# Kernel tuning notes

Measured on AMD Instinct MI355X. Metric: run time of the kernel, lower is better.

Reference implementation:

```python
import jax, jax.numpy as jnp
import numpy as np

B, T, F, D, NH, HD, WIN = 4, 512, 32, 128, 4, 32, 64
HIDDEN = 4 * D


def _ln(x, g, b, eps=1e-5):
    m = x.mean(-1, keepdims=True)
    v = ((x - m) ** 2).mean(-1, keepdims=True)
    return (x - m) / jnp.sqrt(v + eps) * g + b


def _rope(x):
    # x: [N, T, NH, HD] -- identical rotary applied to every head (matches per-head loop)
    hd = x.shape[-1]
    inv_freq = 1.0 / (10000.0 ** (jnp.arange(0, hd, 2, dtype=jnp.float32) / hd))
    t = jnp.arange(x.shape[1], dtype=jnp.float32)
    fr = t[:, None] * inv_freq                      # [T, HD/2]
    sin = jnp.sin(fr)[None, :, None, :]
    cos = jnp.cos(fr)[None, :, None, :]
    xe, xo = x[..., 0::2], x[..., 1::2]
    re = xe * cos - xo * sin
    ro = xe * sin + xo * cos
    return jnp.stack([re, ro], axis=-1).reshape(x.shape)


def setup_inputs() -> dict:
    key = jax.random.key(0)
    ks = jax.random.split(key, 8)
    s = 0.05
    return {
        "x": jax.random.normal(ks[0], (B, T, F), jnp.float32),
        "W_in": jax.random.normal(ks[1], (D, F), jnp.float32) * s,
        "b_in": jnp.zeros((D,), jnp.float32),
        "gamma1": jnp.ones((D,), jnp.float32),
        "beta1": jnp.zeros((D,), jnp.float32),
        "gamma2": jnp.ones((D,), jnp.float32),
        "beta2": jnp.zeros((D,), jnp.float32),
        "W_qkv": jax.random.normal(ks[2], (3 * D, D), jnp.float32) * s,
        "b_qkv": jnp.zeros((3 * D,), jnp.float32),
        "W_o": jax.random.normal(ks[3], (D, D), jnp.float32) * s,
        "b_o": jnp.zeros((D,), jnp.float32),
        "W1": jax.random.normal(ks[4], (HIDDEN, D), jnp.float32) * s,
        "b1": jnp.zeros((HIDDEN,), jnp.float32),
        "W2": jax.random.normal(ks[5], (D, HIDDEN), jnp.float32) * s,
        "b2": jnp.zeros((D,), jnp.float32),
        "W_out": jax.random.normal(ks[6], (F, D), jnp.float32) * s,
        "b_out": jnp.zeros((F,), jnp.float32),
    }


def reference(x, W_in, b_in, gamma1, beta1, gamma2, beta2, W_qkv, b_qkv,
              W_o, b_o, W1, b1, W2, b2, W_out, b_out):
    Bb, Tt, Ff = x.shape
    # channel-independent projection: hcf[b,f,t,:] = x[b,t,f] * W_in[:,f] + b_in
    hcf = jnp.einsum('btf,df->bftd', x, W_in) + b_in        # [B,F,T,D]
    hcf = hcf.reshape(Bb * Ff, Tt, D)                       # [BF,T,D]
    h1 = _ln(hcf, gamma1, beta1)
    # RoPE on q,k BEFORE the attention's internal qkv projection (as in source)
    qk = _rope(h1.reshape(Bb * Ff, Tt, NH, HD)).reshape(Bb * Ff, Tt, D)
    Wq, Wk, Wv = jnp.split(W_qkv, 3, axis=0)
    bq, bk, bv = jnp.split(b_qkv, 3)
    Q = (qk @ Wq.T + bq).reshape(-1, Tt, NH, HD)
    K = (qk @ Wk.T + bk).reshape(-1, Tt, NH, HD)
    V = (h1 @ Wv.T + bv).reshape(-1, Tt, NH, HD)
    i = jnp.arange(Tt)
    allowed = (i[None, :] <= i[:, None]) & ((i[:, None] - i[None, :]) <= WIN)
    mask = jnp.where(allowed, 0.0, -jnp.inf)                # [T,T]
    scores = jnp.einsum('bthd,bshd->bhts', Q, K) / jnp.sqrt(jnp.float32(HD)) + mask
    p = jax.nn.softmax(scores, axis=-1)
    o = jnp.einsum('bhts,bshd->bthd', p, V).reshape(-1, Tt, D)
    y = o @ W_o.T + b_o
    h2 = hcf + y
    h3 = _ln(h2, gamma2, beta2)
    ffn = jax.nn.gelu(h3 @ W1.T + b1, approximate=False) @ W2.T + b2
    h4 = h2 + ffn
    y_out = h4.reshape(Bb, Ff, Tt, D).mean(-1).transpose(0, 2, 1)   # [B,T,F]
    y_proj = (x @ W_in.T + b_in) @ W_out.T + b_out                   # [B,T,F]
    return x + y_out + y_proj
```

## Files before the change

kernel.cpp:

```cpp
#include <hip/hip_runtime.h>
#include <hip/hip_bf16.h>

typedef unsigned short u16;
typedef unsigned int u32;
typedef __attribute__((ext_vector_type(8))) short bf16x8;
typedef __attribute__((ext_vector_type(8))) unsigned short u16x8;
typedef __attribute__((ext_vector_type(4))) float f32x4;
typedef __attribute__((ext_vector_type(4))) unsigned short u16x4;

static constexpr int TSEQ = 512;
static constexpr int NSEQ = 128;
static constexpr int NTOK = NSEQ * TSEQ;

__device__ __forceinline__ float bf2f(u16 u) {
  u32 i = ((u32)u) << 16; float f; __builtin_memcpy(&f, &i, 4); return f;
}
__device__ __forceinline__ u16 f2bf(float f) {
  u32 u; __builtin_memcpy(&u, &f, 4);
  return (u16)((u + 0x7FFFu + ((u >> 16) & 1u)) >> 16);
}
__device__ __forceinline__ f32x4 mfma16(bf16x8 a, bf16x8 b, f32x4 c) {
  return __builtin_amdgcn_mfma_f32_16x16x32_bf16(a, b, c, 0, 0, 0);
}
__device__ __forceinline__ void gload_lds16(const u16* g, u16* l) {
  __builtin_amdgcn_global_load_lds((const __attribute__((address_space(1))) void*)g,
                                   (__attribute__((address_space(3))) void*)l, 16, 0, 0);
}
__device__ __forceinline__ float gelu_t(float v) {
  float uu = 0.7978845608f * (v + 0.044715f * v * v * v);
  return v * __builtin_amdgcn_rcpf(1.f + __expf(-2.f * uu));
}

__global__ void k0_prep(const float* __restrict__ Wqkv, const float* __restrict__ Wo,
                        const float* __restrict__ W1, const float* __restrict__ W2,
                        const float* __restrict__ b2,
                        const float* __restrict__ W_in, const float* __restrict__ b_in,
                        const float* __restrict__ Wout, const float* __restrict__ bout,
                        u16* __restrict__ Wqkv_b, u16* __restrict__ Wo_b,
                        u16* __restrict__ W1_b, float* __restrict__ cm,
                        float* __restrict__ b2m,
                        float* __restrict__ Wcomb, float* __restrict__ bcomb,
                        float* __restrict__ rc, float* __restrict__ rs) {
  int i = blockIdx.x * 256 + threadIdx.x;
  if (i < 49152) Wqkv_b[i] = f2bf(Wqkv[i]);
  if (i < 16384) Wo_b[i] = f2bf(Wo[i]);
  if (i < 65536) W1_b[i] = f2bf(W1[i]);
  if (i < 512) {
    float s = 0.f;
    for (int d = 0; d < 128; ++d) s += W2[d * 512 + i];
    cm[i] = s * (1.f / 128.f);
  }
  if (i == 0) {
    float s = 0.f;
    for (int d = 0; d < 128; ++d) s += b2[d];
    *b2m = s * (1.f / 128.f);
  }
  if (i < 1024) {
    int l = i >> 5, f = i & 31;
    float s = 0.f;
    for (int d = 0; d < 128; ++d) s += Wout[l * 128 + d] * W_in[d * 32 + f];
    Wcomb[i] = s;
  }
  if (i < 32) {
    float s = bout[i];
    for (int d = 0; d < 128; ++d) s += Wout[i * 128 + d] * b_in[d];
    bcomb[i] = s;
  }
  if (i < 8192) {
    int t = i >> 4, fi = i & 15;
    float inv = powf(10000.f, -(float)(2 * fi) / 32.f);
    float ang = (float)t * inv;
    rc[i] = cosf(ang); rs[i] = sinf(ang);
  }
}

__global__ __launch_bounds__(512, 4)
void embed_qkv(const float* __restrict__ x, const float* __restrict__ W_in,
               const float* __restrict__ b_in,
               const float* __restrict__ g1, const float* __restrict__ be1,
               const float* __restrict__ rc, const float* __restrict__ rs,
               const u16* __restrict__ Wqkv, const float* __restrict__ bqkv,
               u16* __restrict__ QKb, u16* __restrict__ Vb) {
  __shared__ u16 Aq[64 * 128];
  __shared__ u16 Ah[64 * 128];
  const int tid = threadIdx.x, l = tid & 63, w = tid >> 6;
  const int lr = l & 15, lg = l >> 4;
  const int m0 = blockIdx.x * 64;
  const int seq = m0 >> 9, f = seq & 31, b = seq >> 5, tbase = m0 & 511;

  {
    const int tok = tid >> 3, j = tid & 7, d0 = j * 16;
    const int t = tbase + tok;
    float xv = x[((b << 9) + t) * 32 + f];
    float hc[16], av[16];
    float s = 0.f, ss = 0.f;
    #pragma unroll
    for (int m = 0; m < 16; ++m) {
      float v = xv * W_in[(d0 + m) * 32 + f] + b_in[d0 + m];
      hc[m] = v; s += v; ss += v * v;
    }
    s += __shfl_xor(s, 1); ss += __shfl_xor(ss, 1);
    s += __shfl_xor(s, 2); ss += __shfl_xor(ss, 2);
    s += __shfl_xor(s, 4); ss += __shfl_xor(ss, 4);
    float mean = s * (1.f / 128.f);
    float var = ss * (1.f / 128.f) - mean * mean;
    float rstd = rsqrtf(var + 1e-5f);
    #pragma unroll
    for (int m = 0; m < 16; ++m)
      av[m] = (hc[m] - mean) * rstd * g1[d0 + m] + be1[d0 + m];
    u16x8 ah0, ah1, aq0, aq1;
    #pragma unroll
    for (int m = 0; m < 8; ++m) { ah0[m] = f2bf(av[m]); ah1[m] = f2bf(av[8 + m]); }
    #pragma unroll
    for (int m = 0; m < 8; ++m) {
      int i16 = ((d0 >> 1) + m) & 15;
      float c = rc[t * 16 + i16], sn = rs[t * 16 + i16];
      float re = av[2 * m] * c - av[2 * m + 1] * sn;
      float ro = av[2 * m] * sn + av[2 * m + 1] * c;
      if (m < 4) { aq0[2 * m] = f2bf(re); aq0[2 * m + 1] = f2bf(ro); }
      else { aq1[2 * (m - 4)] = f2bf(re); aq1[2 * (m - 4) + 1] = f2bf(ro); }
    }
    const int p0 = j * 2;
    const int s0 = p0 ^ (tok & 7), s1 = (p0 + 1) ^ (tok & 7);
    *(u16x8*)(Ah + (tok * 16 + s0) * 8) = ah0;
    *(u16x8*)(Ah + (tok * 16 + s1) * 8) = ah1;
    *(u16x8*)(Aq + (tok * 16 + s0) * 8) = aq0;
    *(u16x8*)(Aq + (tok * 16 + s1) * 8) = aq1;
  }
  __syncthreads();

  #pragma unroll 1
  for (int ph = 0; ph < 3; ++ph) {
    const u16* As = (ph == 2) ? Ah : Aq;
    const int wrow = ph * 128 + w * 16;
    const u16* wr = Wqkv + (size_t)(wrow + lr) * 128 + lg * 8;
    bf16x8 wf0 = *(const bf16x8*)(wr);
    bf16x8 wf1 = *(const bf16x8*)(wr + 32);
    bf16x8 wf2 = *(const bf16x8*)(wr + 64);
    bf16x8 wf3 = *(const bf16x8*)(wr + 96);
    f32x4 bs = *(const f32x4*)(bqkv + wrow + lg * 4);
    u16* C = (ph == 2) ? Vb : QKb;
    const int ldc = (ph == 2) ? 128 : 256;
    const int ccol = ((ph == 2) ? 0 : ph * 128) + w * 16 + lg * 4;
    #pragma unroll
    for (int tt = 0; tt < 4; ++tt) {
      const int tok = tt * 16 + lr;
      const u16* ar = As + (tok * 16) * 8;
      f32x4 a0 = mfma16(wf0, *(const bf16x8*)(ar + ((lg ^ (lr & 7)) << 3)),
                        (f32x4){0.f, 0.f, 0.f, 0.f});
      a0 = mfma16(wf1, *(const bf16x8*)(ar + (((4 + lg) ^ (lr & 7)) << 3)), a0);
      f32x4 a1 = mfma16(wf2, *(const bf16x8*)(ar + (((8 + lg) ^ (lr & 7)) << 3)),
                        (f32x4){0.f, 0.f, 0.f, 0.f});
      a1 = mfma16(wf3, *(const bf16x8*)(ar + (((12 + lg) ^ (lr & 7)) << 3)), a1);
      f32x4 a = a0 + a1;
      u16x4 qv;
      #pragma unroll
      for (int r = 0; r < 4; ++r) qv[r] = f2bf(a[r] + bs[r]);
      *(u16x4*)(C + (size_t)(m0 + tok) * ldc + ccol) = qv;
    }
    __builtin_amdgcn_sched_barrier(0);
  }
}

__global__ __launch_bounds__(512, 4)
void wo_ln_ffn(const u16* __restrict__ OB, const u16* __restrict__ Wo_b,
               const float* __restrict__ bo,
               const float* __restrict__ x, const float* __restrict__ W_in,
               const float* __restrict__ b_in,
               const float* __restrict__ g2, const float* __restrict__ be2,
               const u16* __restrict__ W1b, const float* __restrict__ b1,
               const float* __restrict__ cm, const float* __restrict__ b2m,
               float* __restrict__ yout) {
  __shared__ u16 Buf[64 * 136];
  __shared__ float Sm[64 * 9], Sq[64 * 9];
  __shared__ float Yp[64 * 9];
  __shared__ float Hm[64];
  __shared__ float Xs[64];
  const int tid = threadIdx.x, l = tid & 63, w = tid >> 6;
  const int lr = l & 15, lg = l >> 4;
  const int m0 = blockIdx.x * 64;
  const int seq = m0 >> 9, f = seq & 31, b = seq >> 5, tbase = m0 & 511;
  const int wb = __builtin_amdgcn_readfirstlane(tid & 0x1C0);

  #pragma unroll
  for (int it = 0; it < 2; ++it) {
    int ci = it * 512 + tid;
    int row = ci >> 4, p = ci & 15;
    gload_lds16(OB + (size_t)(m0 + row) * 128 + ((p ^ (row & 7)) << 3),
                Buf + (size_t)(it * 512 + wb) * 8);
  }
  if (tid < 64) Xs[tid] = x[((b << 9) + tbase + tid) * 32 + f];
  __syncthreads();

  const int wrow = w * 16;
  {
    const u16* wr0 = Wo_b + (size_t)(wrow + lr) * 128 + lg * 8;
    bf16x8 wf0 = *(const bf16x8*)(wr0);
    bf16x8 wf1 = *(const bf16x8*)(wr0 + 32);
    bf16x8 wf2 = *(const bf16x8*)(wr0 + 64);
    bf16x8 wf3 = *(const bf16x8*)(wr0 + 96);
    f32x4 bs = *(const f32x4*)(bo + wrow + lg * 4);
    f32x4 winc, binc;
    #pragma unroll
    for (int r = 0; r < 4; ++r) {
      winc[r] = W_in[(wrow + lg * 4 + r) * 32 + f];
      binc[r] = b_in[wrow + lg * 4 + r];
    }
    f32x4 hv[4];
    #pragma unroll
    for (int tt = 0; tt < 4; ++tt) {
      const int tok = tt * 16 + lr;
      const u16* ar = Buf + (tok * 16) * 8;
      f32x4 a0 = mfma16(wf0, *(const bf16x8*)(ar + ((lg ^ (lr & 7)) << 3)),
                        (f32x4){0.f, 0.f, 0.f, 0.f});
      a0 = mfma16(wf1, *(const bf16x8*)(ar + (((4 + lg) ^ (lr & 7)) << 3)), a0);
      f32x4 a1 = mfma16(wf2, *(const bf16x8*)(ar + (((8 + lg) ^ (lr & 7)) << 3)),
                        (f32x4){0.f, 0.f, 0.f, 0.f});
      a1 = mfma16(wf3, *(const bf16x8*)(ar + (((12 + lg) ^ (lr & 7)) << 3)), a1);
      f32x4 a = a0 + a1;
      float xv = Xs[tok];
      #pragma unroll
      for (int r = 0; r < 4; ++r)
        hv[tt][r] = a[r] + bs[r] + (xv * winc[r] + binc[r]);
    }
    #pragma unroll
    for (int tt = 0; tt < 4; ++tt) {
      float psm = hv[tt][0] + hv[tt][1] + hv[tt][2] + hv[tt][3];
      float psq = hv[tt][0] * hv[tt][0] + hv[tt][1] * hv[tt][1]
                + hv[tt][2] * hv[tt][2] + hv[tt][3] * hv[tt][3];
      psm += __shfl_xor(psm, 16); psq += __shfl_xor(psq, 16);
      psm += __shfl_xor(psm, 32); psq += __shfl_xor(psq, 32);
      if (lg == 0) { Sm[(tt * 16 + lr) * 9 + w] = psm; Sq[(tt * 16 + lr) * 9 + w] = psq; }
    }
    __syncthreads();
    f32x4 gm = *(const f32x4*)(g2 + wrow + lg * 4);
    f32x4 bt = *(const f32x4*)(be2 + wrow + lg * 4);
    #pragma unroll
    for (int tt = 0; tt < 4; ++tt) {
      const int tok = tt * 16 + lr;
      float s = 0.f, q = 0.f;
      #pragma unroll
      for (int ww = 0; ww < 8; ++ww) { s += Sm[tok * 9 + ww]; q += Sq[tok * 9 + ww]; }
      float mean = s * (1.f / 128.f);
      float var = q * (1.f / 128.f) - mean * mean;
      float rstd = rsqrtf(var + 1e-5f);
      if (w == 0 && lg == 0) Hm[tok] = mean;
      u16x4 qv;
      #pragma unroll
      for (int r = 0; r < 4; ++r)
        qv[r] = f2bf((hv[tt][r] - mean) * rstd * gm[r] + bt[r]);
      *(u16x4*)(Buf + tok * 136 + wrow + lg * 4) = qv;
    }
  }
  __syncthreads();

  float yacc[4] = {0.f, 0.f, 0.f, 0.f};
  #pragma unroll 1
  for (int p = 0; p < 4; ++p) {
    const int hb = (p * 8 + w) * 16;
    const u16* wr = W1b + (size_t)(hb + lr) * 128 + lg * 8;
    bf16x8 wf0 = *(const bf16x8*)(wr);
    bf16x8 wf1 = *(const bf16x8*)(wr + 32);
    bf16x8 wf2 = *(const bf16x8*)(wr + 64);
    bf16x8 wf3 = *(const bf16x8*)(wr + 96);
    f32x4 cmv = *(const f32x4*)(cm + hb + lg * 4);
    f32x4 bsv = *(const f32x4*)(b1 + hb + lg * 4);
    #pragma unroll
    for (int tt = 0; tt < 4; ++tt) {
      const u16* ar = Buf + (tt * 16 + lr) * 136 + lg * 8;
      f32x4 a0 = mfma16(wf0, *(const bf16x8*)(ar), (f32x4){0.f, 0.f, 0.f, 0.f});
      a0 = mfma16(wf1, *(const bf16x8*)(ar + 32), a0);
      f32x4 a1 = mfma16(wf2, *(const bf16x8*)(ar + 64), (f32x4){0.f, 0.f, 0.f, 0.f});
      a1 = mfma16(wf3, *(const bf16x8*)(ar + 96), a1);
      f32x4 a = a0 + a1;
      #pragma unroll
      for (int r = 0; r < 4; ++r)
        yacc[tt] += cmv[r] * gelu_t(a[r] + bsv[r]);
    }
    __builtin_amdgcn_sched_barrier(0);
  }

  #pragma unroll
  for (int tt = 0; tt < 4; ++tt) {
    float p = yacc[tt];
    p += __shfl_xor(p, 16);
    p += __shfl_xor(p, 32);
    if (lg == 0) Yp[(tt * 16 + lr) * 9 + w] = p;
  }
  __syncthreads();
  if (tid < 64) {
    float s = 0.f;
    #pragma unroll
    for (int ww = 0; ww < 8; ++ww) s += Yp[tid * 9 + ww];
    yout[m0 + tid] = Hm[tid] + b2m[0] + s;
  }
}

__global__ __launch_bounds__(256, 4)
void attn_mfma(const u16* __restrict__ QK, const u16* __restrict__ V, u16* __restrict__ O) {
  __shared__ u16 Ks[192 * 32];
  __shared__ u16 Vt[32 * 192];
  __shared__ u16 Pl[4][16 * 96];
  typedef __attribute__((ext_vector_type(2))) unsigned int u32x2;
  const int qstart = blockIdx.x * 128, seq = blockIdx.y, h = blockIdx.z;
  const int tid = threadIdx.x, w = tid >> 6, l = tid & 63;
  const int lr = l & 15, lg = l >> 4;
  const size_t base = (size_t)seq * TSEQ;

  #pragma unroll
  for (int it = 0; it < 3; ++it) {
    int idx = it * 256 + tid;
    int kl = idx >> 2, c = idx & 3;
    int kg = qstart - 64 + kl; if (kg < 0) kg = 0;
    bf16x8 kv = *(const bf16x8*)(QK + (base + kg) * 256 + 128 + h * 32 + c * 8);
    int pc = c ^ ((kl >> 1) & 3);
    *(bf16x8*)(Ks + kl * 32 + pc * 8) = kv;
    bf16x8 vv = *(const bf16x8*)(V + (base + kg) * 128 + h * 32 + c * 8);
    #pragma unroll
    for (int j = 0; j < 8; ++j) {
      int hd = c * 8 + j;
      int f = ((hd & 7) ^ (hd >> 3)) & 7;
      Vt[hd * 192 + (((kl >> 3) ^ f) * 8) + (kl & 7)] = (u16)vv[j];
    }
  }
  __syncthreads();

  const float scale = 0.17677669529663687f;
  for (int qt = 0; qt < 2; ++qt) {
    const int klbase = (w * 2 + qt) * 16;
    const int t0 = qstart + klbase;
    bf16x8 qf = *(const bf16x8*)(QK + (base + t0 + lr) * 256 + h * 32 + lg * 8);
    f32x4 s[5];
    #pragma unroll
    for (int kt = 0; kt < 5; ++kt) {
      int key = klbase + kt * 16 + lr;
      int pc = lg ^ ((key >> 1) & 3);
      bf16x8 kf = *(const bf16x8*)(Ks + key * 32 + pc * 8);
      s[kt] = mfma16(kf, qf, (f32x4){0.f, 0.f, 0.f, 0.f});
    }
    float m = -1e30f;
    #pragma unroll
    for (int kt = 0; kt < 5; ++kt)
      #pragma unroll
      for (int r = 0; r < 4; ++r) {
        int kl = kt * 16 + lg * 4 + r;
        bool valid = (kl >= lr) && (kl <= lr + 64) && (kl >= 64 - t0);
        float sv = valid ? s[kt][r] * scale : -1e30f;
        s[kt][r] = sv;
        m = fmaxf(m, sv);
      }
    m = fmaxf(m, __shfl_xor(m, 16));
    m = fmaxf(m, __shfl_xor(m, 32));
    float sum = 0.f;
    #pragma unroll
    for (int kt = 0; kt < 5; ++kt)
      #pragma unroll
      for (int r = 0; r < 4; ++r) { float p = __expf(s[kt][r] - m); s[kt][r] = p; sum += p; }
    sum += __shfl_xor(sum, 16);
    sum += __shfl_xor(sum, 32);
    float rinv = 1.f / sum;
    u16* P = Pl[w];
    #pragma unroll
    for (int kt = 0; kt < 5; ++kt) {
      u32 lo = (u32)f2bf(s[kt][0] * rinv) | ((u32)f2bf(s[kt][1] * rinv) << 16);
      u32 hi = (u32)f2bf(s[kt][2] * rinv) | ((u32)f2bf(s[kt][3] * rinv) << 16);
      int u = 2 * kt + (lg >> 1);
      int up = (u & ~3) | ((u & 3) ^ (lr & 3));
      *(u32x2*)(P + lr * 96 + up * 8 + (lg & 1) * 4) = (u32x2){lo, hi};
    }
    {
      int u = 10 + (lg >> 1);
      int up = (u & ~3) | ((u & 3) ^ (lr & 3));
      *(u32x2*)(P + lr * 96 + up * 8 + (lg & 1) * 4) = (u32x2){0u, 0u};
    }
    f32x4 acc[2] = {{0.f,0.f,0.f,0.f},{0.f,0.f,0.f,0.f}};
    #pragma unroll
    for (int c = 0; c < 3; ++c) {
      int u = 4 * c + (lg ^ (lr & 3));
      bf16x8 pf = *(const bf16x8*)(P + lr * 96 + u * 8);
      #pragma unroll
      for (int n = 0; n < 2; ++n) {
        int hd = n * 16 + lr;
        int f = ((hd & 7) ^ (hd >> 3)) & 7;
        int uv = (klbase >> 3) + 4 * c + lg; if (uv > 23) uv = 23;
        bf16x8 vf = *(const bf16x8*)(Vt + hd * 192 + ((uv ^ f) * 8));
        acc[n] = mfma16(pf, vf, acc[n]);
      }
    }
    #pragma unroll
    for (int n = 0; n < 2; ++n)
      #pragma unroll
      for (int r = 0; r < 4; ++r)
        O[(base + t0 + lg * 4 + r) * 128 + h * 32 + n * 16 + lr] = f2bf(acc[n][r]);
  }
}

__global__ void k7_out(const float* __restrict__ x, const float* __restrict__ Wcomb,
                       const float* __restrict__ bcomb, const float* __restrict__ yout,
                       float* __restrict__ out) {
  __shared__ float Wc[32 * 33];
  __shared__ float bc[32];
  const int tid = threadIdx.x;
  for (int i = tid; i < 1024; i += 256) Wc[(i >> 5) * 33 + (i & 31)] = Wcomb[i];
  if (tid < 32) bc[tid] = bcomb[tid];
  __syncthreads();
  const int p = blockIdx.x * 8 + (tid >> 5);
  const int l = tid & 31;
  const int bb = p >> 9, t = p & 511;
  float xv = x[(size_t)p * 32 + l];
  float acc = bc[l];
  #pragma unroll
  for (int ff = 0; ff < 32; ++ff) {
    float xf = __shfl(xv, ff, 32);
    acc += xf * Wc[l * 33 + ff];
  }
  float yo = yout[((bb * 32 + l) << 9) + t];
  out[(size_t)p * 32 + l] = xv + yo + acc;
}

extern "C" void kernel_launch(void* const* d_in, const int* in_sizes, int n_in,
                              void* d_out, int out_size, void* d_ws, size_t ws_size,
                              hipStream_t stream) {
  const float* x    = (const float*)d_in[0];
  const float* W_in = (const float*)d_in[1];
  const float* b_in = (const float*)d_in[2];
  const float* g1   = (const float*)d_in[3];
  const float* be1  = (const float*)d_in[4];
  const float* g2   = (const float*)d_in[5];
  const float* be2  = (const float*)d_in[6];
  const float* Wqkv = (const float*)d_in[7];
  const float* bqkv = (const float*)d_in[8];
  const float* Wo   = (const float*)d_in[9];
  const float* bo   = (const float*)d_in[10];
  const float* W1   = (const float*)d_in[11];
  const float* b1   = (const float*)d_in[12];
  const float* W2   = (const float*)d_in[13];
  const float* b2   = (const float*)d_in[14];
  const float* Wout = (const float*)d_in[15];
  const float* bout = (const float*)d_in[16];
  float* out = (float*)d_out;

  char* ws = (char*)d_ws;
  size_t off = 0;
  auto alloc = [&](size_t bytes) -> void* {
    void* p = ws + off; off += (bytes + 1023) & ~(size_t)1023; return p;
  };
  float* rc     = (float*)alloc(512 * 16 * 4);
  float* rs     = (float*)alloc(512 * 16 * 4);
  u16* Wqkv_b   = (u16*)alloc(49152 * 2);
  u16* Wo_b     = (u16*)alloc(16384 * 2);
  u16* W1_b     = (u16*)alloc(65536 * 2);
  float* cm     = (float*)alloc(512 * 4);
  float* b2m    = (float*)alloc(4);
  float* Wcomb  = (float*)alloc(1024 * 4);
  float* bcomb  = (float*)alloc(32 * 4);
  float* yout   = (float*)alloc((size_t)NTOK * 4);
  u16* obuf     = (u16*)alloc((size_t)NTOK * 128 * 2);
  u16* QKb      = (u16*)alloc((size_t)NTOK * 256 * 2);
  u16* Vb       = (u16*)alloc((size_t)NTOK * 128 * 2);

  k0_prep<<<dim3(256), dim3(256), 0, stream>>>(Wqkv, Wo, W1, W2, b2,
                                               W_in, b_in, Wout, bout,
                                               Wqkv_b, Wo_b, W1_b, cm, b2m,
                                               Wcomb, bcomb, rc, rs);
  embed_qkv<<<dim3(1024), dim3(512), 0, stream>>>(x, W_in, b_in, g1, be1, rc, rs,
                                                  Wqkv_b, bqkv, QKb, Vb);
  attn_mfma<<<dim3(4, 128, 4), dim3(256), 0, stream>>>(QKb, Vb, obuf);
  wo_ln_ffn<<<dim3(1024), dim3(512), 0, stream>>>(obuf, Wo_b, bo, x, W_in, b_in,
                                                  g2, be2, W1_b, b1, cm, b2m, yout);
  k7_out<<<dim3(256), dim3(256), 0, stream>>>(x, Wcomb, bcomb, yout, out);
}
```

Measured before the change: 112.7 us.

## Shrink wo_ln_ffn token tile to 32 with 4 waves per block

Reworks the fused Wo+LayerNorm+FFN kernel to process 32 tokens per block with 256 threads instead of 64 tokens with 512 threads, launching twice as many blocks. Each wave now covers two 16-row output-channel chunks in the Wo stage and walks 8 hidden chunks instead of 4 in the FFN stage. The aim is smaller LDS per block, more resident blocks and finer scheduling granularity. In exchange, W1 and Wo weight fragments are reloaded per 32 tokens rather than per 64, which doubles weight traffic per token.

```diff
diff --git a/kernel.cpp b/kernel.cpp
--- a/kernel.cpp
+++ b/kernel.cpp
@@ -162,7 +162,7 @@
   }
 }
 
-__global__ __launch_bounds__(512, 4)
+__global__ __launch_bounds__(256, 4)
 void wo_ln_ffn(const u16* __restrict__ OB, const u16* __restrict__ Wo_b,
                const float* __restrict__ bo,
                const float* __restrict__ x, const float* __restrict__ W_in,
@@ -171,29 +171,31 @@
                const u16* __restrict__ W1b, const float* __restrict__ b1,
                const float* __restrict__ cm, const float* __restrict__ b2m,
                float* __restrict__ yout) {
-  __shared__ u16 Buf[64 * 136];
-  __shared__ float Sm[64 * 9], Sq[64 * 9];
-  __shared__ float Yp[64 * 9];
-  __shared__ float Hm[64];
-  __shared__ float Xs[64];
+  __shared__ u16 Buf[32 * 136];
+  __shared__ float Sm[32 * 5], Sq[32 * 5];
+  __shared__ float Yp[32 * 5];
+  __shared__ float Hm[32];
+  __shared__ float Xs[32];
   const int tid = threadIdx.x, l = tid & 63, w = tid >> 6;
   const int lr = l & 15, lg = l >> 4;
-  const int m0 = blockIdx.x * 64;
+  const int m0 = blockIdx.x * 32;
   const int seq = m0 >> 9, f = seq & 31, b = seq >> 5, tbase = m0 & 511;
-  const int wb = __builtin_amdgcn_readfirstlane(tid & 0x1C0);
+  const int wb = __builtin_amdgcn_readfirstlane(tid & 0xC0);
 
   #pragma unroll
   for (int it = 0; it < 2; ++it) {
-    int ci = it * 512 + tid;
+    int ci = it * 256 + tid;
     int row = ci >> 4, p = ci & 15;
     gload_lds16(OB + (size_t)(m0 + row) * 128 + ((p ^ (row & 7)) << 3),
-                Buf + (size_t)(it * 512 + wb) * 8);
-  }
-  if (tid < 64) Xs[tid] = x[((b << 9) + tbase + tid) * 32 + f];
-  __syncthreads();
-
-  const int wrow = w * 16;
-  {
+                Buf + (size_t)(it * 256 + wb) * 8);
+  }
+  if (tid < 32) Xs[tid] = x[((b << 9) + tbase + tid) * 32 + f];
+  __syncthreads();
+
+  f32x4 hvs[2][2];
+  #pragma unroll
+  for (int ch = 0; ch < 2; ++ch) {
+    const int wrow = w * 32 + ch * 16;
     const u16* wr0 = Wo_b + (size_t)(wrow + lr) * 128 + lg * 8;
     bf16x8 wf0 = *(const bf16x8*)(wr0);
     bf16x8 wf1 = *(const bf16x8*)(wr0 + 32);
@@ -206,9 +208,8 @@
       winc[r] = W_in[(wrow + lg * 4 + r) * 32 + f];
       binc[r] = b_in[wrow + lg * 4 + r];
     }
-    f32x4 hv[4];
-    #pragma unroll
-    for (int tt = 0; tt < 4; ++tt) {
+    #pragma unroll
+    for (int tt = 0; tt < 2; ++tt) {
       const int tok = tt * 16 + lr;
       const u16* ar = Buf + (tok * 16) * 8;
       f32x4 a0 = mfma16(wf0, *(const bf16x8*)(ar + ((lg ^ (lr & 7)) << 3)),
@@ -221,43 +222,52 @@
       float xv = Xs[tok];
       #pragma unroll
       for (int r = 0; r < 4; ++r)
-        hv[tt][r] = a[r] + bs[r] + (xv * winc[r] + binc[r]);
-    }
-    #pragma unroll
-    for (int tt = 0; tt < 4; ++tt) {
-      float psm = hv[tt][0] + hv[tt][1] + hv[tt][2] + hv[tt][3];
-      float psq = hv[tt][0] * hv[tt][0] + hv[tt][1] * hv[tt][1]
-                + hv[tt][2] * hv[tt][2] + hv[tt][3] * hv[tt][3];
-      psm += __shfl_xor(psm, 16); psq += __shfl_xor(psq, 16);
-      psm += __shfl_xor(psm, 32); psq += __shfl_xor(psq, 32);
-      if (lg == 0) { Sm[(tt * 16 + lr) * 9 + w] = psm; Sq[(tt * 16 + lr) * 9 + w] = psq; }
-    }
-    __syncthreads();
-    f32x4 gm = *(const f32x4*)(g2 + wrow + lg * 4);
-    f32x4 bt = *(const f32x4*)(be2 + wrow + lg * 4);
-    #pragma unroll
-    for (int tt = 0; tt < 4; ++tt) {
-      const int tok = tt * 16 + lr;
-      float s = 0.f, q = 0.f;
-      #pragma unroll
-      for (int ww = 0; ww < 8; ++ww) { s += Sm[tok * 9 + ww]; q += Sq[tok * 9 + ww]; }
-      float mean = s * (1.f / 128.f);
-      float var = q * (1.f / 128.f) - mean * mean;
-      float rstd = rsqrtf(var + 1e-5f);
-      if (w == 0 && lg == 0) Hm[tok] = mean;
+        hvs[ch][tt][r] = a[r] + bs[r] + (xv * winc[r] + binc[r]);
+    }
+  }
+  #pragma unroll
+  for (int tt = 0; tt < 2; ++tt) {
+    float pm = 0.f, pq = 0.f;
+    #pragma unroll
+    for (int ch = 0; ch < 2; ++ch)
+      #pragma unroll
+      for (int r = 0; r < 4; ++r) {
+        float v = hvs[ch][tt][r];
+        pm += v; pq += v * v;
+      }
+    pm += __shfl_xor(pm, 16); pq += __shfl_xor(pq, 16);
+    pm += __shfl_xor(pm, 32); pq += __shfl_xor(pq, 32);
+    if (lg == 0) { Sm[(tt * 16 + lr) * 5 + w] = pm; Sq[(tt * 16 + lr) * 5 + w] = pq; }
+  }
+  __syncthreads();
+  #pragma unroll
+  for (int tt = 0; tt < 2; ++tt) {
+    const int tok = tt * 16 + lr;
+    float s = 0.f, q = 0.f;
+    #pragma unroll
+    for (int ww = 0; ww < 4; ++ww) { s += Sm[tok * 5 + ww]; q += Sq[tok * 5 + ww]; }
+    float mean = s * (1.f / 128.f);
+    float var = q * (1.f / 128.f) - mean * mean;
+    float rstd = rsqrtf(var + 1e-5f);
+    if (w == 0 && lg == 0) Hm[tok] = mean;
+    #pragma unroll
+    for (int ch = 0; ch < 2; ++ch) {
+      const int wrow = w * 32 + ch * 16;
+      f32x4 gm = *(const f32x4*)(g2 + wrow + lg * 4);
+      f32x4 bt = *(const f32x4*)(be2 + wrow + lg * 4);
       u16x4 qv;
       #pragma unroll
       for (int r = 0; r < 4; ++r)
-        qv[r] = f2bf((hv[tt][r] - mean) * rstd * gm[r] + bt[r]);
+        qv[r] = f2bf((hvs[ch][tt][r] - mean) * rstd * gm[r] + bt[r]);
       *(u16x4*)(Buf + tok * 136 + wrow + lg * 4) = qv;
     }
   }
   __syncthreads();
 
-  float yacc[4] = {0.f, 0.f, 0.f, 0.f};
+  float yacc[2] = {0.f, 0.f};
   #pragma unroll 1
-  for (int p = 0; p < 4; ++p) {
-    const int hb = (p * 8 + w) * 16;
+  for (int p = 0; p < 8; ++p) {
+    const int hb = (p * 4 + w) * 16;
     const u16* wr = W1b + (size_t)(hb + lr) * 128 + lg * 8;
     bf16x8 wf0 = *(const bf16x8*)(wr);
     bf16x8 wf1 = *(const bf16x8*)(wr + 32);
@@ -266,7 +276,7 @@
     f32x4 cmv = *(const f32x4*)(cm + hb + lg * 4);
     f32x4 bsv = *(const f32x4*)(b1 + hb + lg * 4);
     #pragma unroll
-    for (int tt = 0; tt < 4; ++tt) {
+    for (int tt = 0; tt < 2; ++tt) {
       const u16* ar = Buf + (tt * 16 + lr) * 136 + lg * 8;
       f32x4 a0 = mfma16(wf0, *(const bf16x8*)(ar), (f32x4){0.f, 0.f, 0.f, 0.f});
       a0 = mfma16(wf1, *(const bf16x8*)(ar + 32), a0);
@@ -281,17 +291,17 @@
   }
 
   #pragma unroll
-  for (int tt = 0; tt < 4; ++tt) {
+  for (int tt = 0; tt < 2; ++tt) {
     float p = yacc[tt];
     p += __shfl_xor(p, 16);
     p += __shfl_xor(p, 32);
-    if (lg == 0) Yp[(tt * 16 + lr) * 9 + w] = p;
-  }
-  __syncthreads();
-  if (tid < 64) {
+    if (lg == 0) Yp[(tt * 16 + lr) * 5 + w] = p;
+  }
+  __syncthreads();
+  if (tid < 32) {
     float s = 0.f;
     #pragma unroll
-    for (int ww = 0; ww < 8; ++ww) s += Yp[tid * 9 + ww];
+    for (int ww = 0; ww < 4; ++ww) s += Yp[tid * 5 + ww];
     yout[m0 + tid] = Hm[tid] + b2m[0] + s;
   }
 }
@@ -466,7 +476,7 @@
   embed_qkv<<<dim3(1024), dim3(512), 0, stream>>>(x, W_in, b_in, g1, be1, rc, rs,
                                                   Wqkv_b, bqkv, QKb, Vb);
   attn_mfma<<<dim3(4, 128, 4), dim3(256), 0, stream>>>(QKb, Vb, obuf);
-  wo_ln_ffn<<<dim3(1024), dim3(512), 0, stream>>>(obuf, Wo_b, bo, x, W_in, b_in,
+  wo_ln_ffn<<<dim3(2048), dim3(256), 0, stream>>>(obuf, Wo_b, bo, x, W_in, b_in,
                                                   g2, be2, W1_b, b1, cm, b2m, yout);
   k7_out<<<dim3(256), dim3(256), 0, stream>>>(x, Wcomb, bcomb, yout, out);
 }
```

Result: slower. 128.7 us (+14.2%).
